# Kernel tuning notes

Hardware: AMD Instinct MI355X
Metric: run time of the kernel (lower is better)

The kernel has to match this reference:

```python
import jax, jax.numpy as jnp
import numpy as np

LN_EPS = 1e-5

def _layer_norm(x, g, b):
    mu = jnp.mean(x, axis=-1, keepdims=True)
    var = jnp.var(x, axis=-1, keepdims=True)
    return (x - mu) * jax.lax.rsqrt(var + LN_EPS) * g + b

def _mlp(x, W1, b1, g1, beta1, W2, b2):
    h = x @ W1 + b1
    h = _layer_norm(h, g1, beta1)
    h = jax.nn.silu(h)
    return h @ W2 + b2

def setup_inputs() -> dict:
    key = jax.random.key(0)
    ks = jax.random.split(key, 16)
    N, E = 50000, 600000
    node_dim, edge_dim, hidden = 128, 128, 256
    def lin(k, fan_in, fan_out):
        bound = 1.0 / np.sqrt(fan_in)
        kw, kb = jax.random.split(k)
        W = jax.random.uniform(kw, (fan_in, fan_out), jnp.float32, -bound, bound)
        b = jax.random.uniform(kb, (fan_out,), jnp.float32, -bound, bound)
        return W, b
    eW1, eb1 = lin(ks[0], 2 * node_dim + edge_dim, hidden)
    eW2, eb2 = lin(ks[1], hidden, edge_dim)
    nW1, nb1 = lin(ks[2], node_dim + edge_dim, hidden)
    nW2, nb2 = lin(ks[3], hidden, node_dim)
    return {
        "node_features": jax.random.normal(ks[4], (N, node_dim), jnp.float32),
        "edge_features": jax.random.normal(ks[5], (E, edge_dim), jnp.float32),
        "edge_index": jax.random.randint(ks[6], (2, E), 0, N, jnp.int64),
        "eW1": eW1, "eb1": eb1, "eg1": jnp.ones((hidden,), jnp.float32), "ebeta1": jnp.zeros((hidden,), jnp.float32),
        "eW2": eW2, "eb2": eb2,
        "nW1": nW1, "nb1": nb1, "ng1": jnp.ones((hidden,), jnp.float32), "nbeta1": jnp.zeros((hidden,), jnp.float32),
        "nW2": nW2, "nb2": nb2,
    }

def reference(node_features, edge_features, edge_index,
              eW1, eb1, eg1, ebeta1, eW2, eb2,
              nW1, nb1, ng1, nbeta1, nW2, nb2):
    senders = edge_index[0]
    receivers = edge_index[1]
    # gather -> edge MLP (residual)
    edge_input = jnp.concatenate(
        [node_features[senders], node_features[receivers], edge_features], axis=-1)  # [E, 2*nd+ed]
    edge_features = edge_features + _mlp(edge_input, eW1, eb1, eg1, ebeta1, eW2, eb2)
    # scatter-add aggregate over receivers
    n_nodes = node_features.shape[0]
    aggregated = jax.ops.segment_sum(edge_features, receivers, num_segments=n_nodes)
    # node MLP (residual)
    node_input = jnp.concatenate([node_features, aggregated], axis=-1)  # [N, nd+ed]
    node_features = node_features + _mlp(node_input, nW1, nb1, ng1, nbeta1, nW2, nb2)
    return node_features, edge_features
```

## Files before the change

kernel.cpp:

```cpp
#include <hip/hip_runtime.h>

#define N_NODES 50000
#define N_EDGES 600000
#define DIM 128
#define HID 256
#define MR 32

typedef float  f32x4  __attribute__((ext_vector_type(4), aligned(16), may_alias));
typedef float  f32x2  __attribute__((ext_vector_type(2), aligned(8),  may_alias));
typedef __bf16 bf16x8 __attribute__((ext_vector_type(8), aligned(16), may_alias));

static __device__ inline f32x4 mfma16x16x32(bf16x8 a, bf16x8 b, f32x4 c) {
    return __builtin_amdgcn_mfma_f32_16x16x32_bf16(a, b, c, 0, 0, 0);
}

static __device__ inline bf16x8 load8_f32_to_bf16(const float* __restrict__ p) {
    f32x4 a = *(const f32x4*)p;
    f32x4 b = *(const f32x4*)(p + 4);
    bf16x8 o;
    o[0] = (__bf16)a[0]; o[1] = (__bf16)a[1]; o[2] = (__bf16)a[2]; o[3] = (__bf16)a[3];
    o[4] = (__bf16)b[0]; o[5] = (__bf16)b[1]; o[6] = (__bf16)b[2]; o[7] = (__bf16)b[3];
    return o;
}

__global__ void pack_kernel(const float* __restrict__ W, __bf16* __restrict__ out,
                            int K, int Ncols) {
    int idx = blockIdx.x * 256 + threadIdx.x;
    int total = (K >> 5) * (Ncols >> 4) * 64;
    if (idx >= total) return;
    int lane = idx & 63;
    int tc = idx >> 6;
    int nC = Ncols >> 4;
    int c = tc % nC;
    int t = tc / nC;
    int col = (c << 4) + (lane & 15);
    int k0 = (t << 5) + ((lane >> 4) << 3);
    bf16x8 v;
#pragma unroll
    for (int j = 0; j < 8; ++j) v[j] = (__bf16)W[(k0 + j) * Ncols + col];
    *((bf16x8*)out + idx) = v;
}

__global__ void hist_kernel(const int* __restrict__ eidx, int* __restrict__ counts) {
    int e = blockIdx.x * 256 + threadIdx.x;
    if (e < N_EDGES) {
        int r = eidx[N_EDGES + e];
        r = (r < 0) ? 0 : (r >= N_NODES ? N_NODES - 1 : r);
        atomicAdd(&counts[r], 1);
    }
}

__global__ __launch_bounds__(1024) void scan_kernel(const int* __restrict__ counts,
                                                    int* __restrict__ offsets,
                                                    int* __restrict__ cursor) {
    __shared__ int part[1024];
    const int t = threadIdx.x;
    const int CH = (N_NODES + 1023) / 1024;
    const int base = t * CH;
    int s = 0;
#pragma unroll 1
    for (int i = 0; i < CH; ++i) {
        int idx = base + i;
        if (idx < N_NODES) s += counts[idx];
    }
    part[t] = s;
    __syncthreads();
    for (int d = 1; d < 1024; d <<= 1) {
        int x = (t >= d) ? part[t - d] : 0;
        __syncthreads();
        part[t] += x;
        __syncthreads();
    }
    int run = part[t] - s;
#pragma unroll 1
    for (int i = 0; i < CH; ++i) {
        int idx = base + i;
        if (idx < N_NODES) {
            offsets[idx] = run;
            cursor[idx]  = run;
            run += counts[idx];
        }
    }
    if (t == 1023) offsets[N_NODES] = run;
}

__global__ void scatter_kernel(const int* __restrict__ eidx,
                               int* __restrict__ cursor, int* __restrict__ eids) {
    int e = blockIdx.x * 256 + threadIdx.x;
    if (e < N_EDGES) {
        int r = eidx[N_EDGES + e];
        r = (r < 0) ? 0 : (r >= N_NODES ? N_NODES - 1 : r);
        int pos = atomicAdd(&cursor[r], 1);
        eids[pos] = e;
    }
}

template<int ASTRIDE, int T1>
__device__ inline void mlp_core(char* lds,
                                const bf16x8* __restrict__ pW1,
                                const bf16x8* __restrict__ pW2,
                                const float* __restrict__ b1,
                                const float* __restrict__ g1,
                                const float* __restrict__ be1,
                                f32x4 (&acc2)[2][2]) {
    const int tid = threadIdx.x;
    const int w = tid >> 6;
    const int lane = tid & 63;
    const int l16 = lane & 15;
    const int g = lane >> 4;
    float* stats = (float*)(lds + 32 * ASTRIDE);

    f32x4 acc[2][4];
#pragma unroll
    for (int m = 0; m < 2; ++m)
#pragma unroll
        for (int n = 0; n < 4; ++n) acc[m][n] = (f32x4){0.f, 0.f, 0.f, 0.f};
#pragma unroll
    for (int t = 0; t < T1; ++t) {
        bf16x8 af[2];
#pragma unroll
        for (int m = 0; m < 2; ++m)
            af[m] = *(const bf16x8*)(lds + (m * 16 + l16) * ASTRIDE + t * 64 + g * 16);
        const bf16x8* bp = pW1 + ((t * 16 + 4 * w) << 6) + lane;
#pragma unroll
        for (int n = 0; n < 4; ++n) {
            bf16x8 bf = bp[n << 6];
#pragma unroll
            for (int m = 0; m < 2; ++m)
                acc[m][n] = mfma16x16x32(af[m], bf, acc[m][n]);
        }
    }

    float b1v[4];
#pragma unroll
    for (int n = 0; n < 4; ++n) b1v[n] = b1[64 * w + 16 * n + l16];
#pragma unroll
    for (int m = 0; m < 2; ++m)
#pragma unroll
        for (int r = 0; r < 4; ++r) {
            float s = 0.f, q = 0.f;
#pragma unroll
            for (int n = 0; n < 4; ++n) {
                float x = acc[m][n][r] + b1v[n];
                acc[m][n][r] = x;
                s += x; q += x * x;
            }
            s += __shfl_xor(s, 1); q += __shfl_xor(q, 1);
            s += __shfl_xor(s, 2); q += __shfl_xor(q, 2);
            s += __shfl_xor(s, 4); q += __shfl_xor(q, 4);
            s += __shfl_xor(s, 8); q += __shfl_xor(q, 8);
            if (l16 == 0) {
                int row = m * 16 + g * 4 + r;
                *(f32x2*)(stats + row * 8 + w * 2) = (f32x2){s, q};
            }
        }
    __syncthreads();

    float mu[2][4], rs[2][4];
#pragma unroll
    for (int m = 0; m < 2; ++m)
#pragma unroll
        for (int r = 0; r < 4; ++r) {
            int row = m * 16 + g * 4 + r;
            f32x4 a = *(const f32x4*)(stats + row * 8);
            f32x4 b = *(const f32x4*)(stats + row * 8 + 4);
            float S = (a[0] + a[2]) + (b[0] + b[2]);
            float Q = (a[1] + a[3]) + (b[1] + b[3]);
            float mm = S * (1.f / 256.f);
            float vv = fmaxf(Q * (1.f / 256.f) - mm * mm, 0.f);
            mu[m][r] = mm;
            rs[m][r] = rsqrtf(vv + 1e-5f);
        }
    float g1v[4], bev[4];
#pragma unroll
    for (int n = 0; n < 4; ++n) {
        g1v[n] = g1[64 * w + 16 * n + l16];
        bev[n] = be1[64 * w + 16 * n + l16];
    }
#pragma unroll
    for (int m = 0; m < 2; ++m)
#pragma unroll
        for (int n = 0; n < 4; ++n)
#pragma unroll
            for (int r = 0; r < 4; ++r) {
                float x = (acc[m][n][r] - mu[m][r]) * rs[m][r] * g1v[n] + bev[n];
                x = x / (1.f + __expf(-x));
                int row = m * 16 + g * 4 + r;
                int col = 64 * w + 16 * n + l16;
                *(__bf16*)(lds + row * 528 + col * 2) = (__bf16)x;
            }
    __syncthreads();

#pragma unroll
    for (int m = 0; m < 2; ++m)
#pragma unroll
        for (int n = 0; n < 2; ++n) acc2[m][n] = (f32x4){0.f, 0.f, 0.f, 0.f};
#pragma unroll
    for (int t = 0; t < 8; ++t) {
        bf16x8 af[2];
#pragma unroll
        for (int m = 0; m < 2; ++m)
            af[m] = *(const bf16x8*)(lds + (m * 16 + l16) * 528 + t * 64 + g * 16);
        const bf16x8* bp = pW2 + ((t * 8 + 2 * w) << 6) + lane;
#pragma unroll
        for (int n = 0; n < 2; ++n) {
            bf16x8 bf = bp[n << 6];
#pragma unroll
            for (int m = 0; m < 2; ++m)
                acc2[m][n] = mfma16x16x32(af[m], bf, acc2[m][n]);
        }
    }
}

__global__ __launch_bounds__(256, 5) void edge_kernel(
    const float* __restrict__ node, const float* __restrict__ ef,
    const int* __restrict__ eidx,
    const bf16x8* __restrict__ pW1, const bf16x8* __restrict__ pW2,
    const float* __restrict__ b1, const float* __restrict__ g1,
    const float* __restrict__ be1, const float* __restrict__ b2,
    float* __restrict__ out_edges) {
    __shared__ __align__(16) char lds[MR * 784 + MR * 32];
    const int tid = threadIdx.x;
    const int eb = blockIdx.x * MR;

    {
        int row = tid >> 3, l8 = tid & 7;
        int e = eb + row;
        int snd = eidx[e], rcv = eidx[N_EDGES + e];
        snd = (snd < 0) ? 0 : (snd >= N_NODES ? N_NODES - 1 : snd);
        rcv = (rcv < 0) ? 0 : (rcv >= N_NODES ? N_NODES - 1 : rcv);
        const float* ps = node + (size_t)snd * DIM;
        const float* pr = node + (size_t)rcv * DIM;
        const float* pe = ef + (size_t)e * DIM;
#pragma unroll
        for (int i = 0; i < 6; ++i) {
            int c = l8 + (i << 3);
            const float* src = (c < 16) ? (ps + (c << 3))
                             : (c < 32) ? (pr + ((c - 16) << 3))
                                        : (pe + ((c - 32) << 3));
            *(bf16x8*)(lds + row * 784 + (c << 4)) = load8_f32_to_bf16(src);
        }
    }
    __syncthreads();

    f32x4 acc2[2][2];
    mlp_core<784, 12>(lds, pW1, pW2, b1, g1, be1, acc2);

    {
        const int w = tid >> 6, lane = tid & 63;
        const int l16 = lane & 15, g = lane >> 4;
        float b2v[2];
#pragma unroll
        for (int n = 0; n < 2; ++n) b2v[n] = b2[32 * w + 16 * n + l16];
#pragma unroll
        for (int m = 0; m < 2; ++m)
#pragma unroll
            for (int n = 0; n < 2; ++n)
#pragma unroll
                for (int r = 0; r < 4; ++r) {
                    int e = eb + m * 16 + g * 4 + r;
                    int col = 32 * w + 16 * n + l16;
                    size_t off = (size_t)e * DIM + col;
                    out_edges[off] = acc2[m][n][r] + b2v[n] + ef[off];
                }
    }
}

__global__ __launch_bounds__(256, 5) void node_kernel(
    const float* __restrict__ node, const float* __restrict__ out_edges,
    const int* __restrict__ offsets, const int* __restrict__ eids,
    const bf16x8* __restrict__ pW1, const bf16x8* __restrict__ pW2,
    const float* __restrict__ b1, const float* __restrict__ g1,
    const float* __restrict__ be1, const float* __restrict__ b2,
    float* __restrict__ out_nodes) {
    __shared__ __align__(16) char lds[MR * 528 + MR * 32];
    const int tid = threadIdx.x;
    const int nb = blockIdx.x * MR;

    {
        int row = tid >> 3, l8 = tid & 7;
        int n = nb + row;
        int nc = (n > N_NODES - 1) ? N_NODES - 1 : n;
#pragma unroll
        for (int i = 0; i < 2; ++i) {
            int c = l8 + (i << 3);
            *(bf16x8*)(lds + row * 528 + (c << 4)) =
                load8_f32_to_bf16(node + (size_t)nc * DIM + (c << 3));
        }
        float a[16];
#pragma unroll
        for (int j = 0; j < 16; ++j) a[j] = 0.f;
        int st = offsets[nc], en = offsets[nc + 1];
#pragma unroll 1
        for (int i = st; i < en; ++i) {
            int e = eids[i];
            const float* er = out_edges + (size_t)e * DIM + (l8 << 4);
#pragma unroll
            for (int k = 0; k < 4; ++k) {
                f32x4 v = *(const f32x4*)(er + (k << 2));
                a[k * 4 + 0] += v[0]; a[k * 4 + 1] += v[1];
                a[k * 4 + 2] += v[2]; a[k * 4 + 3] += v[3];
            }
        }
        bf16x8 o0, o1;
#pragma unroll
        for (int j = 0; j < 8; ++j) { o0[j] = (__bf16)a[j]; o1[j] = (__bf16)a[8 + j]; }
        int cbase = 16 + (l8 << 1);
        *(bf16x8*)(lds + row * 528 + (cbase << 4)) = o0;
        *(bf16x8*)(lds + row * 528 + ((cbase + 1) << 4)) = o1;
    }
    __syncthreads();

    f32x4 acc2[2][2];
    mlp_core<528, 8>(lds, pW1, pW2, b1, g1, be1, acc2);

    {
        const int w = tid >> 6, lane = tid & 63;
        const int l16 = lane & 15, g = lane >> 4;
        float b2v[2];
#pragma unroll
        for (int n = 0; n < 2; ++n) b2v[n] = b2[32 * w + 16 * n + l16];
#pragma unroll
        for (int m = 0; m < 2; ++m)
#pragma unroll
            for (int n = 0; n < 2; ++n)
#pragma unroll
                for (int r = 0; r < 4; ++r) {
                    int nd = nb + m * 16 + g * 4 + r;
                    if (nd < N_NODES) {
                        int col = 32 * w + 16 * n + l16;
                        size_t off = (size_t)nd * DIM + col;
                        out_nodes[off] = acc2[m][n][r] + b2v[n] + node[off];
                    }
                }
    }
}

extern "C" void kernel_launch(void* const* d_in, const int* in_sizes, int n_in,
                              void* d_out, int out_size, void* d_ws, size_t ws_size,
                              hipStream_t stream) {
    const float* node  = (const float*)d_in[0];
    const float* ef    = (const float*)d_in[1];
    const int*   eidx  = (const int*)d_in[2];
    const float* eW1   = (const float*)d_in[3];
    const float* eb1   = (const float*)d_in[4];
    const float* eg1   = (const float*)d_in[5];
    const float* ebt1  = (const float*)d_in[6];
    const float* eW2   = (const float*)d_in[7];
    const float* eb2   = (const float*)d_in[8];
    const float* nW1   = (const float*)d_in[9];
    const float* nb1   = (const float*)d_in[10];
    const float* ng1   = (const float*)d_in[11];
    const float* nbt1  = (const float*)d_in[12];
    const float* nW2   = (const float*)d_in[13];
    const float* nb2   = (const float*)d_in[14];

    char* ws = (char*)d_ws;
    int* counts  = (int*)ws;
    int* offsets = counts + 50016;
    int* cursor  = offsets + 50016;
    int* eids    = cursor + 50016;
    char* wbase = (char*)(eids + 600064);
    __bf16* peW1 = (__bf16*)(((uintptr_t)wbase + 255) & ~(uintptr_t)255);
    __bf16* peW2 = peW1 + 384 * 256;
    __bf16* pnW1 = peW2 + 256 * 128;
    __bf16* pnW2 = pnW1 + 256 * 256;

    hipMemsetAsync(counts, 0, 50000 * sizeof(int), stream);
    pack_kernel<<<48, 256, 0, stream>>>(eW1, peW1, 384, 256);
    pack_kernel<<<16, 256, 0, stream>>>(eW2, peW2, 256, 128);
    pack_kernel<<<32, 256, 0, stream>>>(nW1, pnW1, 256, 256);
    pack_kernel<<<16, 256, 0, stream>>>(nW2, pnW2, 256, 128);

    hist_kernel<<<(N_EDGES + 255) / 256, 256, 0, stream>>>(eidx, counts);
    scan_kernel<<<1, 1024, 0, stream>>>(counts, offsets, cursor);
    scatter_kernel<<<(N_EDGES + 255) / 256, 256, 0, stream>>>(eidx, cursor, eids);

    float* out_nodes = (float*)d_out;
    float* out_edges = out_nodes + (size_t)N_NODES * DIM;

    edge_kernel<<<N_EDGES / MR, 256, 0, stream>>>(
        node, ef, eidx, (const bf16x8*)peW1, (const bf16x8*)peW2,
        eb1, eg1, ebt1, eb2, out_edges);
    node_kernel<<<(N_NODES + MR - 1) / MR, 256, 0, stream>>>(
        node, out_edges, offsets, eids, (const bf16x8*)pnW1, (const bf16x8*)pnW2,
        nb1, ng1, nbt1, nb2, out_nodes);
}
```

Before: 653.5 us.

## Prefetch weight fragments, swizzle hidden LDS tile, unroll CSR gather, raise occupancy

Both GEMM loops in the shared MLP core now software-pipeline the global weight-fragment loads, fetching the next k-step's B operands while issuing MFMAs on the current ones. The hidden-activation LDS tile gets an XOR swizzle on write and read to cut bank conflicts. The node kernel's segment-sum gather loop is unrolled by two so two edge rows are in flight at once. Launch bounds rise from 5 to 6 blocks per SM, which tightens the register budget and risks spills, especially with the extra prefetch registers.

```diff
diff --git a/kernel.cpp b/kernel.cpp
--- a/kernel.cpp
+++ b/kernel.cpp
@@ -115,19 +115,30 @@
     for (int m = 0; m < 2; ++m)
 #pragma unroll
         for (int n = 0; n < 4; ++n) acc[m][n] = (f32x4){0.f, 0.f, 0.f, 0.f};
+    bf16x8 bc[4];
+    {
+        const bf16x8* bp = pW1 + ((4 * w) << 6) + lane;
+#pragma unroll
+        for (int n = 0; n < 4; ++n) bc[n] = bp[n << 6];
+    }
 #pragma unroll
     for (int t = 0; t < T1; ++t) {
-        bf16x8 af[2];
-#pragma unroll
-        for (int m = 0; m < 2; ++m)
-            af[m] = *(const bf16x8*)(lds + (m * 16 + l16) * ASTRIDE + t * 64 + g * 16);
-        const bf16x8* bp = pW1 + ((t * 16 + 4 * w) << 6) + lane;
+        bf16x8 af0 = *(const bf16x8*)(lds + l16 * ASTRIDE + t * 64 + g * 16);
+        bf16x8 af1 = *(const bf16x8*)(lds + (16 + l16) * ASTRIDE + t * 64 + g * 16);
+        bf16x8 bn[4];
+        if (t + 1 < T1) {
+            const bf16x8* bp = pW1 + (((t + 1) * 16 + 4 * w) << 6) + lane;
+#pragma unroll
+            for (int n = 0; n < 4; ++n) bn[n] = bp[n << 6];
+        }
 #pragma unroll
         for (int n = 0; n < 4; ++n) {
-            bf16x8 bf = bp[n << 6];
-#pragma unroll
-            for (int m = 0; m < 2; ++m)
-                acc[m][n] = mfma16x16x32(af[m], bf, acc[m][n]);
+            acc[0][n] = mfma16x16x32(af0, bc[n], acc[0][n]);
+            acc[1][n] = mfma16x16x32(af1, bc[n], acc[1][n]);
+        }
+        if (t + 1 < T1) {
+#pragma unroll
+            for (int n = 0; n < 4; ++n) bc[n] = bn[n];
         }
     }
 
@@ -177,6 +188,7 @@
         g1v[n] = g1[64 * w + 16 * n + l16];
         bev[n] = be1[64 * w + 16 * n + l16];
     }
+    const int wswz = g << 4;
 #pragma unroll
     for (int m = 0; m < 2; ++m)
 #pragma unroll
@@ -187,7 +199,7 @@
                 x = x / (1.f + __expf(-x));
                 int row = m * 16 + g * 4 + r;
                 int col = 64 * w + 16 * n + l16;
-                *(__bf16*)(lds + row * 528 + col * 2) = (__bf16)x;
+                *(__bf16*)(lds + ((row * 528 + col * 2) ^ wswz)) = (__bf16)x;
             }
     __syncthreads();
 
@@ -195,24 +207,30 @@
     for (int m = 0; m < 2; ++m)
 #pragma unroll
         for (int n = 0; n < 2; ++n) acc2[m][n] = (f32x4){0.f, 0.f, 0.f, 0.f};
+    const int rsw = (l16 & 12) << 2;
+    bf16x8 c0, c1;
+    {
+        const bf16x8* bp = pW2 + ((2 * w) << 6) + lane;
+        c0 = bp[0]; c1 = bp[1 << 6];
+    }
 #pragma unroll
     for (int t = 0; t < 8; ++t) {
-        bf16x8 af[2];
-#pragma unroll
-        for (int m = 0; m < 2; ++m)
-            af[m] = *(const bf16x8*)(lds + (m * 16 + l16) * 528 + t * 64 + g * 16);
-        const bf16x8* bp = pW2 + ((t * 8 + 2 * w) << 6) + lane;
-#pragma unroll
-        for (int n = 0; n < 2; ++n) {
-            bf16x8 bf = bp[n << 6];
-#pragma unroll
-            for (int m = 0; m < 2; ++m)
-                acc2[m][n] = mfma16x16x32(af[m], bf, acc2[m][n]);
-        }
-    }
-}
-
-__global__ __launch_bounds__(256, 5) void edge_kernel(
+        bf16x8 af0 = *(const bf16x8*)(lds + ((l16 * 528 + t * 64 + g * 16) ^ rsw));
+        bf16x8 af1 = *(const bf16x8*)(lds + (((16 + l16) * 528 + t * 64 + g * 16) ^ rsw));
+        bf16x8 n0, n1;
+        if (t < 7) {
+            const bf16x8* bp = pW2 + (((t + 1) * 8 + 2 * w) << 6) + lane;
+            n0 = bp[0]; n1 = bp[1 << 6];
+        }
+        acc2[0][0] = mfma16x16x32(af0, c0, acc2[0][0]);
+        acc2[1][0] = mfma16x16x32(af1, c0, acc2[1][0]);
+        acc2[0][1] = mfma16x16x32(af0, c1, acc2[0][1]);
+        acc2[1][1] = mfma16x16x32(af1, c1, acc2[1][1]);
+        if (t < 7) { c0 = n0; c1 = n1; }
+    }
+}
+
+__global__ __launch_bounds__(256, 6) void edge_kernel(
     const float* __restrict__ node, const float* __restrict__ ef,
     const int* __restrict__ eidx,
     const bf16x8* __restrict__ pW1, const bf16x8* __restrict__ pW2,
@@ -266,7 +284,7 @@
     }
 }
 
-__global__ __launch_bounds__(256, 5) void node_kernel(
+__global__ __launch_bounds__(256, 6) void node_kernel(
     const float* __restrict__ node, const float* __restrict__ out_edges,
     const int* __restrict__ offsets, const int* __restrict__ eids,
     const bf16x8* __restrict__ pW1, const bf16x8* __restrict__ pW2,
@@ -291,13 +309,30 @@
 #pragma unroll
         for (int j = 0; j < 16; ++j) a[j] = 0.f;
         int st = offsets[nc], en = offsets[nc + 1];
+        int i = st;
 #pragma unroll 1
-        for (int i = st; i < en; ++i) {
-            int e = eids[i];
-            const float* er = out_edges + (size_t)e * DIM + (l8 << 4);
+        for (; i + 2 <= en; i += 2) {
+            int e0 = eids[i], e1 = eids[i + 1];
+            const float* er0 = out_edges + (size_t)e0 * DIM + (l8 << 4);
+            const float* er1 = out_edges + (size_t)e1 * DIM + (l8 << 4);
+            f32x4 u0 = ((const f32x4*)er0)[0], u1 = ((const f32x4*)er0)[1];
+            f32x4 u2 = ((const f32x4*)er0)[2], u3 = ((const f32x4*)er0)[3];
+            f32x4 v0 = ((const f32x4*)er1)[0], v1 = ((const f32x4*)er1)[1];
+            f32x4 v2 = ((const f32x4*)er1)[2], v3 = ((const f32x4*)er1)[3];
 #pragma unroll
             for (int k = 0; k < 4; ++k) {
-                f32x4 v = *(const f32x4*)(er + (k << 2));
+                a[0 + k] += u0[k] + v0[k];
+                a[4 + k] += u1[k] + v1[k];
+                a[8 + k] += u2[k] + v2[k];
+                a[12 + k] += u3[k] + v3[k];
+            }
+        }
+        if (i < en) {
+            int e0 = eids[i];
+            const float* er0 = out_edges + (size_t)e0 * DIM + (l8 << 4);
+#pragma unroll
+            for (int k = 0; k < 4; ++k) {
+                f32x4 v = ((const f32x4*)er0)[k];
                 a[k * 4 + 0] += v[0]; a[k * 4 + 1] += v[1];
                 a[k * 4 + 2] += v[2]; a[k * 4 + 3] += v[3];
             }
```

Result: slower. 687.1 us (+5.1%).

## Pre-convert node features to bf16 and gather bf16 rows in edge kernel

Applied to the files above, without the earlier changes.

Adds a pre-pass that converts node features to a bf16 copy in workspace, so the edge kernel gathers sender/receiver rows at half the bytes and skips per-edge conversion. The four weight-pack launches are merged into one kernel. The node aggregation loop is unrolled by two edges to put more loads in flight, and launch bounds move from 5 to 6 waves per SIMD. The extra pre-pass and workspace traffic are the cost, and the tighter register budget may cause spills.

```diff
diff --git a/kernel.cpp b/kernel.cpp
--- a/kernel.cpp
+++ b/kernel.cpp
@@ -9,25 +9,31 @@
 typedef float  f32x4  __attribute__((ext_vector_type(4), aligned(16), may_alias));
 typedef float  f32x2  __attribute__((ext_vector_type(2), aligned(8),  may_alias));
 typedef __bf16 bf16x8 __attribute__((ext_vector_type(8), aligned(16), may_alias));
+typedef int    i32x4  __attribute__((ext_vector_type(4), aligned(16), may_alias));
 
 static __device__ inline f32x4 mfma16x16x32(bf16x8 a, bf16x8 b, f32x4 c) {
     return __builtin_amdgcn_mfma_f32_16x16x32_bf16(a, b, c, 0, 0, 0);
 }
 
-static __device__ inline bf16x8 load8_f32_to_bf16(const float* __restrict__ p) {
-    f32x4 a = *(const f32x4*)p;
-    f32x4 b = *(const f32x4*)(p + 4);
+static __device__ inline bf16x8 cvt2_bf16(f32x4 a, f32x4 b) {
     bf16x8 o;
     o[0] = (__bf16)a[0]; o[1] = (__bf16)a[1]; o[2] = (__bf16)a[2]; o[3] = (__bf16)a[3];
     o[4] = (__bf16)b[0]; o[5] = (__bf16)b[1]; o[6] = (__bf16)b[2]; o[7] = (__bf16)b[3];
     return o;
 }
 
-__global__ void pack_kernel(const float* __restrict__ W, __bf16* __restrict__ out,
-                            int K, int Ncols) {
+__global__ void nbf_kernel(const float* __restrict__ node, __bf16* __restrict__ nbf) {
     int idx = blockIdx.x * 256 + threadIdx.x;
-    int total = (K >> 5) * (Ncols >> 4) * 64;
-    if (idx >= total) return;
+    if (idx >= N_NODES * 16) return;
+    int row = idx >> 4, c = idx & 15;
+    const float* p = node + (size_t)row * DIM + (c << 3);
+    f32x4 a = ((const f32x4*)p)[0], b = ((const f32x4*)p)[1];
+    *(bf16x8*)(nbf + (size_t)row * DIM + (c << 3)) = cvt2_bf16(a, b);
+}
+
+static __device__ inline void pack_one(const float* __restrict__ W,
+                                       __bf16* __restrict__ out,
+                                       int idx, int Ncols) {
     int lane = idx & 63;
     int tc = idx >> 6;
     int nC = Ncols >> 4;
@@ -39,6 +45,17 @@
 #pragma unroll
     for (int j = 0; j < 8; ++j) v[j] = (__bf16)W[(k0 + j) * Ncols + col];
     *((bf16x8*)out + idx) = v;
+}
+
+__global__ void pack_all_kernel(const float* __restrict__ eW1, const float* __restrict__ eW2,
+                                const float* __restrict__ nW1, const float* __restrict__ nW2,
+                                __bf16* __restrict__ peW1, __bf16* __restrict__ peW2,
+                                __bf16* __restrict__ pnW1, __bf16* __restrict__ pnW2) {
+    int idx = blockIdx.x * 256 + threadIdx.x;
+    if (idx < 12288)       pack_one(eW1, peW1, idx, 256);
+    else if (idx < 16384)  pack_one(eW2, peW2, idx - 12288, 128);
+    else if (idx < 24576)  pack_one(nW1, pnW1, idx - 16384, 256);
+    else                   pack_one(nW2, pnW2, idx - 24576, 128);
 }
 
 __global__ void hist_kernel(const int* __restrict__ eidx, int* __restrict__ counts) {
@@ -212,8 +229,8 @@
     }
 }
 
-__global__ __launch_bounds__(256, 5) void edge_kernel(
-    const float* __restrict__ node, const float* __restrict__ ef,
+__global__ __launch_bounds__(256, 6) void edge_kernel(
+    const __bf16* __restrict__ nbf, const float* __restrict__ ef,
     const int* __restrict__ eidx,
     const bf16x8* __restrict__ pW1, const bf16x8* __restrict__ pW2,
     const float* __restrict__ b1, const float* __restrict__ g1,
@@ -229,17 +246,18 @@
         int snd = eidx[e], rcv = eidx[N_EDGES + e];
         snd = (snd < 0) ? 0 : (snd >= N_NODES ? N_NODES - 1 : snd);
         rcv = (rcv < 0) ? 0 : (rcv >= N_NODES ? N_NODES - 1 : rcv);
-        const float* ps = node + (size_t)snd * DIM;
-        const float* pr = node + (size_t)rcv * DIM;
-        const float* pe = ef + (size_t)e * DIM;
-#pragma unroll
-        for (int i = 0; i < 6; ++i) {
-            int c = l8 + (i << 3);
-            const float* src = (c < 16) ? (ps + (c << 3))
-                             : (c < 32) ? (pr + ((c - 16) << 3))
-                                        : (pe + ((c - 32) << 3));
-            *(bf16x8*)(lds + row * 784 + (c << 4)) = load8_f32_to_bf16(src);
-        }
+        const char* ps = (const char*)(nbf + (size_t)snd * DIM) + (l8 << 5);
+        const char* pr = (const char*)(nbf + (size_t)rcv * DIM) + (l8 << 5);
+        char* dst = lds + row * 784 + (l8 << 5);
+        *(i32x4*)dst         = *(const i32x4*)ps;
+        *(i32x4*)(dst + 16)  = *(const i32x4*)(ps + 16);
+        *(i32x4*)(dst + 256) = *(const i32x4*)pr;
+        *(i32x4*)(dst + 272) = *(const i32x4*)(pr + 16);
+        const float* pe = ef + (size_t)e * DIM + (l8 << 4);
+        f32x4 a0 = ((const f32x4*)pe)[0], a1 = ((const f32x4*)pe)[1];
+        f32x4 a2 = ((const f32x4*)pe)[2], a3 = ((const f32x4*)pe)[3];
+        *(bf16x8*)(dst + 512) = cvt2_bf16(a0, a1);
+        *(bf16x8*)(dst + 528) = cvt2_bf16(a2, a3);
     }
     __syncthreads();
 
@@ -266,8 +284,9 @@
     }
 }
 
-__global__ __launch_bounds__(256, 5) void node_kernel(
-    const float* __restrict__ node, const float* __restrict__ out_edges,
+__global__ __launch_bounds__(256, 6) void node_kernel(
+    const float* __restrict__ node, const __bf16* __restrict__ nbf,
+    const float* __restrict__ out_edges,
     const int* __restrict__ offsets, const int* __restrict__ eids,
     const bf16x8* __restrict__ pW1, const bf16x8* __restrict__ pW2,
     const float* __restrict__ b1, const float* __restrict__ g1,
@@ -281,23 +300,38 @@
         int row = tid >> 3, l8 = tid & 7;
         int n = nb + row;
         int nc = (n > N_NODES - 1) ? N_NODES - 1 : n;
-#pragma unroll
-        for (int i = 0; i < 2; ++i) {
-            int c = l8 + (i << 3);
-            *(bf16x8*)(lds + row * 528 + (c << 4)) =
-                load8_f32_to_bf16(node + (size_t)nc * DIM + (c << 3));
-        }
+        const char* pn = (const char*)(nbf + (size_t)nc * DIM) + (l8 << 5);
+        char* dst = lds + row * 528 + (l8 << 5);
+        *(i32x4*)dst        = *(const i32x4*)pn;
+        *(i32x4*)(dst + 16) = *(const i32x4*)(pn + 16);
         float a[16];
 #pragma unroll
         for (int j = 0; j < 16; ++j) a[j] = 0.f;
         int st = offsets[nc], en = offsets[nc + 1];
+        int i = st;
 #pragma unroll 1
-        for (int i = st; i < en; ++i) {
-            int e = eids[i];
-            const float* er = out_edges + (size_t)e * DIM + (l8 << 4);
+        for (; i + 2 <= en; i += 2) {
+            int e0 = eids[i], e1 = eids[i + 1];
+            const float* er0 = out_edges + (size_t)e0 * DIM + (l8 << 4);
+            const float* er1 = out_edges + (size_t)e1 * DIM + (l8 << 4);
+            f32x4 u0 = ((const f32x4*)er0)[0], u1 = ((const f32x4*)er0)[1];
+            f32x4 u2 = ((const f32x4*)er0)[2], u3 = ((const f32x4*)er0)[3];
+            f32x4 v0 = ((const f32x4*)er1)[0], v1 = ((const f32x4*)er1)[1];
+            f32x4 v2 = ((const f32x4*)er1)[2], v3 = ((const f32x4*)er1)[3];
 #pragma unroll
             for (int k = 0; k < 4; ++k) {
-                f32x4 v = *(const f32x4*)(er + (k << 2));
+                a[0 + k]  += u0[k] + v0[k];
+                a[4 + k]  += u1[k] + v1[k];
+                a[8 + k]  += u2[k] + v2[k];
+                a[12 + k] += u3[k] + v3[k];
+            }
+        }
+        if (i < en) {
+            int e0 = eids[i];
+            const float* er0 = out_edges + (size_t)e0 * DIM + (l8 << 4);
+#pragma unroll
+            for (int k = 0; k < 4; ++k) {
+                f32x4 v = ((const f32x4*)er0)[k];
                 a[k * 4 + 0] += v[0]; a[k * 4 + 1] += v[1];
                 a[k * 4 + 2] += v[2]; a[k * 4 + 3] += v[3];
             }
@@ -360,17 +394,16 @@
     int* offsets = counts + 50016;
     int* cursor  = offsets + 50016;
     int* eids    = cursor + 50016;
-    char* wbase = (char*)(eids + 600064);
-    __bf16* peW1 = (__bf16*)(((uintptr_t)wbase + 255) & ~(uintptr_t)255);
+    char* nbase = (char*)(eids + 600064);
+    __bf16* nbf = (__bf16*)(((uintptr_t)nbase + 255) & ~(uintptr_t)255);
+    __bf16* peW1 = nbf + (size_t)N_NODES * DIM;
     __bf16* peW2 = peW1 + 384 * 256;
     __bf16* pnW1 = peW2 + 256 * 128;
     __bf16* pnW2 = pnW1 + 256 * 256;
 
     hipMemsetAsync(counts, 0, 50000 * sizeof(int), stream);
-    pack_kernel<<<48, 256, 0, stream>>>(eW1, peW1, 384, 256);
-    pack_kernel<<<16, 256, 0, stream>>>(eW2, peW2, 256, 128);
-    pack_kernel<<<32, 256, 0, stream>>>(nW1, pnW1, 256, 256);
-    pack_kernel<<<16, 256, 0, stream>>>(nW2, pnW2, 256, 128);
+    nbf_kernel<<<(N_NODES * 16 + 255) / 256, 256, 0, stream>>>(node, nbf);
+    pack_all_kernel<<<112, 256, 0, stream>>>(eW1, eW2, nW1, nW2, peW1, peW2, pnW1, pnW2);
 
     hist_kernel<<<(N_EDGES + 255) / 256, 256, 0, stream>>>(eidx, counts);
     scan_kernel<<<1, 1024, 0, stream>>>(counts, offsets, cursor);
@@ -380,9 +413,9 @@
     float* out_edges = out_nodes + (size_t)N_NODES * DIM;
 
     edge_kernel<<<N_EDGES / MR, 256, 0, stream>>>(
-        node, ef, eidx, (const bf16x8*)peW1, (const bf16x8*)peW2,
+        nbf, ef, eidx, (const bf16x8*)peW1, (const bf16x8*)peW2,
         eb1, eg1, ebt1, eb2, out_edges);
     node_kernel<<<(N_NODES + MR - 1) / MR, 256, 0, stream>>>(
-        node, out_edges, offsets, eids, (const bf16x8*)pnW1, (const bf16x8*)pnW2,
+        node, nbf, out_edges, offsets, eids, (const bf16x8*)pnW1, (const bf16x8*)pnW2,
         nb1, ng1, nbt1, nb2, out_nodes);
 }
```

Result: slower. 682.4 us (+4.4%).
